# Optimization experiments

Hardware: AMD Instinct MI355X
Metric: run time of the kernel (lower is better)

Reference implementation:

```python
import jax, jax.numpy as jnp
import numpy as np

MARGIN = 0.35


def setup_inputs() -> dict:
    key = jax.random.key(0)
    k1, k2 = jax.random.split(key)
    N, D = 8192, 512
    inp = jax.random.normal(k1, (N, D), dtype=jnp.float32)
    label = jax.random.randint(k2, (N,), 0, D, dtype=jnp.int64)
    return {"input": inp, "label": label}


def reference(input, label):
    N = input.shape[0]
    # Faithful to the torch code: squared-norm terms use L2-normalized input,
    # but the -2*x@x.T cross term uses the UNnormalized input (original quirk).
    x_norm = input / jnp.linalg.norm(input, axis=1, keepdims=True)
    sq = jnp.sum(x_norm * x_norm, axis=1, keepdims=True)  # [N,1]
    dist = sq + sq.T - 2.0 * (input @ input.T)            # [N,N]
    mask = label[:, None] == label[None, :]               # same-label mask
    neg_inf = jnp.array(-jnp.inf, dist.dtype)
    pos_inf = jnp.array(jnp.inf, dist.dtype)
    # hardest positive (max over same-label), hardest negative (min over diff-label)
    positive_part = jnp.max(jnp.where(mask, dist, neg_inf), axis=1)
    negative_part = jnp.min(jnp.where(mask, pos_inf, dist), axis=1)
    triplet = jnp.mean(jnp.maximum(positive_part - negative_part + MARGIN, 0.0))
    # cross entropy: input are logits, label class indices
    logz = jax.nn.logsumexp(input, axis=1)
    true_logit = jnp.take_along_axis(input, label[:, None].astype(jnp.int32), axis=1)[:, 0]
    ce = jnp.mean(logz - true_logit)
    return triplet + ce
```

## Files before the change

kernel.cpp:

```cpp
#include <hip/hip_runtime.h>
#include <hip/hip_bf16.h>
#include <stdint.h>

#define N_ROWS 8192
#define DIM 512
#define NLAB 512
#define MARGIN_F 0.35f
#define NBLK 64
#define NPURE 1953
#define NDIAG 127
#define NTILE (NPURE + NDIAG)
#define ROWSTAT_BLOCKS (N_ROWS / 4)

typedef __attribute__((ext_vector_type(4))) float floatx4;
typedef __attribute__((ext_vector_type(16))) float floatx16;
typedef __attribute__((ext_vector_type(8))) int intx8;

__device__ __forceinline__ unsigned enc_f(float f) {
    unsigned u = __float_as_uint(f);
    return (u & 0x80000000u) ? ~u : (u | 0x80000000u);
}
__device__ __forceinline__ float dec_f(unsigned e) {
    unsigned u = (e & 0x80000000u) ? (e ^ 0x80000000u) : ~e;
    return __uint_as_float(u);
}

__device__ __forceinline__ void load_lds16(const void* g, void* l) {
    __builtin_amdgcn_global_load_lds((__attribute__((address_space(1))) void*)(void*)g,
                                     (__attribute__((address_space(3))) void*)l, 16, 0, 0);
}

__global__ __launch_bounds__(512) void histscan_kernel(const int* __restrict__ label,
                                                       int* __restrict__ offsetArr,
                                                       int* __restrict__ cnt,
                                                       float* __restrict__ out) {
    __shared__ int h[NLAB];
    __shared__ int sc[NLAB];
    int t = threadIdx.x;
    h[t] = 0;
    __syncthreads();
    for (int i = t; i < N_ROWS; i += 512) atomicAdd(&h[label[i]], 1);
    __syncthreads();
    int v = h[t];
    sc[t] = v;
    __syncthreads();
    for (int d = 1; d < NLAB; d <<= 1) {
        int add = (t >= d) ? sc[t - d] : 0;
        __syncthreads();
        sc[t] += add;
        __syncthreads();
    }
    offsetArr[t] = sc[t] - v;
    cnt[t] = 0;
    if (t == 0) out[0] = 0.f;
}

__global__ __launch_bounds__(256) void rowstats_kernel(const float* __restrict__ x,
                                                       const int* __restrict__ label,
                                                       const int* __restrict__ offsetArr,
                                                       int* __restrict__ cnt,
                                                       unsigned char* __restrict__ a8,
                                                       int* __restrict__ sortedLabel,
                                                       float* __restrict__ cePartial,
                                                       unsigned* __restrict__ minEnc,
                                                       unsigned* __restrict__ maxEnc) {
    int gid = blockIdx.x * 256 + threadIdx.x;
    if (gid < N_ROWS) { minEnc[gid] = 0xFFFFFFFFu; maxEnc[gid] = 0u; }

    int w = threadIdx.x >> 6;
    int row = blockIdx.x * 4 + w;
    int l = threadIdx.x & 63;
    const float* xr = x + (size_t)row * DIM;
    float4 v0 = ((const float4*)xr)[2 * l];
    float4 v1 = ((const float4*)xr)[2 * l + 1];
    float vals[8] = {v0.x, v0.y, v0.z, v0.w, v1.x, v1.y, v1.z, v1.w};

    float mx = vals[0];
#pragma unroll
    for (int i = 1; i < 8; i++) mx = fmaxf(mx, vals[i]);
#pragma unroll
    for (int s = 1; s < 64; s <<= 1) mx = fmaxf(mx, __shfl_xor(mx, s, 64));

    float se = 0.f;
#pragma unroll
    for (int i = 0; i < 8; i++) se += expf(vals[i] - mx);
#pragma unroll
    for (int s = 1; s < 64; s <<= 1) se += __shfl_xor(se, s, 64);

    int pos = 0;
    if (l == 0) {
        int lab = label[row];
        pos = offsetArr[lab] + atomicAdd(&cnt[lab], 1);
        sortedLabel[pos] = lab;
    }
    pos = __shfl(pos, 0, 64);

    int w0 = __builtin_amdgcn_cvt_pk_fp8_f32(vals[0], vals[1], 0, false);
    w0 = __builtin_amdgcn_cvt_pk_fp8_f32(vals[2], vals[3], w0, true);
    int w1 = __builtin_amdgcn_cvt_pk_fp8_f32(vals[4], vals[5], 0, false);
    w1 = __builtin_amdgcn_cvt_pk_fp8_f32(vals[6], vals[7], w1, true);
    ((uint2*)(a8 + (size_t)pos * DIM))[l] = make_uint2((unsigned)w0, (unsigned)w1);

    __shared__ float wsum[4];
    if (l == 0) {
        float tl = xr[label[row]];
        wsum[w] = mx + logf(se) - tl;
    }
    __syncthreads();
    if (threadIdx.x == 0)
        cePartial[blockIdx.x] = wsum[0] + wsum[1] + wsum[2] + wsum[3];
}

__global__ __launch_bounds__(256, 4) void gemm_kernel(const unsigned char* __restrict__ A,
                                                      const int* __restrict__ sortedLabel,
                                                      unsigned* __restrict__ minEnc,
                                                      unsigned* __restrict__ maxEnc) {
    __shared__ unsigned char As[2][128 * 64];
    __shared__ unsigned char Bs[2][128 * 64];
    __shared__ float redA[128][2], redB[128][2];
    __shared__ float redImn[128][2], redJmn[128][2];
    __shared__ int labi[128], labj[128];

    int b = blockIdx.x;
    bool diag = (b < NDIAG);
    int bi, bj;
    if (diag) {
        bi = (b < 64) ? b : (b - 63);
        bj = (b < 64) ? b : (b - 64);
    } else {
        int p = b - NDIAG;
        int ci = (int)((sqrtf(8.0f * (float)p + 1.0f) - 1.0f) * 0.5f);
        while ((ci + 1) * (ci + 2) / 2 <= p) ci++;
        while (ci * (ci + 1) / 2 > p) ci--;
        bj = p - ci * (ci + 1) / 2;
        bi = ci + 2;
    }
    int ibase = bi * 128, jbase = bj * 128;

    int t = threadIdx.x;
    int w = t >> 6, l = t & 63;
    int wm = w >> 1, wn = w & 1;
    int cl = l & 31;
    int hi = l >> 5;

    if (diag) {
        if (t < 128) labi[t] = sortedLabel[ibase + t];
        else labj[t - 128] = sortedLabel[jbase + t - 128];
    }

    floatx16 acc[2][2];
#pragma unroll
    for (int a = 0; a < 2; a++)
#pragma unroll
        for (int c = 0; c < 2; c++) acc[a][c] = (floatx16)0.f;

    int s0 = t, s1 = t + 256;
    int r0_ = s0 >> 2, r1_ = s1 >> 2;
    int c0_ = (s0 & 3) ^ ((r0_ >> 1) & 3);
    int c1_ = (s1 & 3) ^ ((r1_ >> 1) & 3);
    const unsigned char* srcA0 = A + (size_t)(ibase + r0_) * DIM + c0_ * 16;
    const unsigned char* srcA1 = A + (size_t)(ibase + r1_) * DIM + c1_ * 16;
    const unsigned char* srcB0 = A + (size_t)(jbase + r0_) * DIM + c0_ * 16;
    const unsigned char* srcB1 = A + (size_t)(jbase + r1_) * DIM + c1_ * 16;
    int ldo0 = s0 * 16, ldo1 = s1 * 16;

#define STAGE(KK, BUF)                                      \
    {                                                       \
        load_lds16(srcA0 + (KK) * 64, As[BUF] + ldo0);      \
        load_lds16(srcA1 + (KK) * 64, As[BUF] + ldo1);      \
        load_lds16(srcB0 + (KK) * 64, Bs[BUF] + ldo0);      \
        load_lds16(srcB1 + (KK) * 64, Bs[BUF] + ldo1);      \
    }

    STAGE(0, 0);
    STAGE(1, 1);
    __syncthreads();

#pragma unroll
    for (int kk = 0; kk < 8; kk++) {
        int cur = kk & 1;

        intx8 b0, b1;
        {
            int r = wn * 64 + cl;
            int f = (r >> 1) & 3;
            const int4* rp = (const int4*)(Bs[cur] + r * 64);
            int4 lo = rp[(2 * hi) ^ f];
            int4 h4 = rp[(2 * hi + 1) ^ f];
            b0[0] = lo.x; b0[1] = lo.y; b0[2] = lo.z; b0[3] = lo.w;
            b0[4] = h4.x; b0[5] = h4.y; b0[6] = h4.z; b0[7] = h4.w;
        }
        {
            int r = wn * 64 + 32 + cl;
            int f = (r >> 1) & 3;
            const int4* rp = (const int4*)(Bs[cur] + r * 64);
            int4 lo = rp[(2 * hi) ^ f];
            int4 h4 = rp[(2 * hi + 1) ^ f];
            b1[0] = lo.x; b1[1] = lo.y; b1[2] = lo.z; b1[3] = lo.w;
            b1[4] = h4.x; b1[5] = h4.y; b1[6] = h4.z; b1[7] = h4.w;
        }
#pragma unroll
        for (int tm = 0; tm < 2; tm++) {
            int r = wm * 64 + tm * 32 + cl;
            int f = (r >> 1) & 3;
            const int4* rp = (const int4*)(As[cur] + r * 64);
            int4 lo = rp[(2 * hi) ^ f];
            int4 h4 = rp[(2 * hi + 1) ^ f];
            intx8 a;
            a[0] = lo.x; a[1] = lo.y; a[2] = lo.z; a[3] = lo.w;
            a[4] = h4.x; a[5] = h4.y; a[6] = h4.z; a[7] = h4.w;
            acc[tm][0] = __builtin_amdgcn_mfma_scale_f32_32x32x64_f8f6f4(
                a, b0, acc[tm][0], 0, 0, 0, 0x7F7F7F7F, 0, 0x7F7F7F7F);
            acc[tm][1] = __builtin_amdgcn_mfma_scale_f32_32x32x64_f8f6f4(
                a, b1, acc[tm][1], 0, 0, 0, 0x7F7F7F7F, 0, 0x7F7F7F7F);
        }

        if (kk < 7) {
            __builtin_amdgcn_s_barrier();
            if (kk < 6) STAGE(kk + 2, cur);
            if (kk < 6) {
                asm volatile("s_waitcnt vmcnt(4)" ::: "memory");
            } else {
                asm volatile("s_waitcnt vmcnt(0)" ::: "memory");
            }
            __builtin_amdgcn_sched_barrier(0);
            __builtin_amdgcn_s_barrier();
        }
    }
#undef STAGE

    const float INF = __builtin_inff();
    int rbase = 4 * hi;

    if (!diag) {
        float mxJ0 = -INF, mxJ1 = -INF;
#pragma unroll
        for (int tm = 0; tm < 2; tm++) {
            float rm[16];
#pragma unroll
            for (int r = 0; r < 16; r++) {
                float v0 = acc[tm][0][r], v1 = acc[tm][1][r];
                rm[r] = fmaxf(v0, v1);
                mxJ0 = fmaxf(mxJ0, v0);
                mxJ1 = fmaxf(mxJ1, v1);
            }
#pragma unroll
            for (int r = 0; r < 16; r++)
#pragma unroll
                for (int s = 1; s < 32; s <<= 1)
                    rm[r] = fmaxf(rm[r], __shfl_xor(rm[r], s, 64));
            if (cl == 0) {
#pragma unroll
                for (int r = 0; r < 16; r++)
                    redA[wm * 64 + tm * 32 + (r & 3) + 8 * (r >> 2) + rbase][wn] = rm[r];
            }
        }
        mxJ0 = fmaxf(mxJ0, __shfl_xor(mxJ0, 32, 64));
        mxJ1 = fmaxf(mxJ1, __shfl_xor(mxJ1, 32, 64));
        if (hi == 0) {
            redB[wn * 64 + cl][wm] = mxJ0;
            redB[wn * 64 + 32 + cl][wm] = mxJ1;
        }
        __syncthreads();
        if (t < 128) {
            atomicMax(&maxEnc[ibase + t], enc_f(fmaxf(redA[t][0], redA[t][1])));
            atomicMax(&maxEnc[jbase + t], enc_f(fmaxf(redB[t][0], redB[t][1])));
        }
    } else {
        int jl0 = labj[wn * 64 + cl];
        int jl1 = labj[wn * 64 + 32 + cl];
        float mnJ0 = INF, mnJ1 = INF, mxJ0 = -INF, mxJ1 = -INF;
#pragma unroll
        for (int tm = 0; tm < 2; tm++) {
            float rmn[16], rmx[16];
#pragma unroll
            for (int r = 0; r < 16; r++) {
                int row_l = wm * 64 + tm * 32 + (r & 3) + 8 * (r >> 2) + rbase;
                int il = labi[row_l];
                float v0 = acc[tm][0][r], v1 = acc[tm][1][r];
                bool sm0 = (jl0 == il), sm1 = (jl1 == il);
                float a0 = sm0 ? v0 : INF, d0 = sm0 ? -INF : v0;
                float a1 = sm1 ? v1 : INF, d1 = sm1 ? -INF : v1;
                rmn[r] = fminf(a0, a1);
                rmx[r] = fmaxf(d0, d1);
                mnJ0 = fminf(mnJ0, a0); mxJ0 = fmaxf(mxJ0, d0);
                mnJ1 = fminf(mnJ1, a1); mxJ1 = fmaxf(mxJ1, d1);
            }
#pragma unroll
            for (int r = 0; r < 16; r++)
#pragma unroll
                for (int s = 1; s < 32; s <<= 1) {
                    rmn[r] = fminf(rmn[r], __shfl_xor(rmn[r], s, 64));
                    rmx[r] = fmaxf(rmx[r], __shfl_xor(rmx[r], s, 64));
                }
            if (cl == 0) {
#pragma unroll
                for (int r = 0; r < 16; r++) {
                    int row_l = wm * 64 + tm * 32 + (r & 3) + 8 * (r >> 2) + rbase;
                    redImn[row_l][wn] = rmn[r];
                    redA[row_l][wn] = rmx[r];
                }
            }
        }
        mnJ0 = fminf(mnJ0, __shfl_xor(mnJ0, 32, 64));
        mnJ1 = fminf(mnJ1, __shfl_xor(mnJ1, 32, 64));
        mxJ0 = fmaxf(mxJ0, __shfl_xor(mxJ0, 32, 64));
        mxJ1 = fmaxf(mxJ1, __shfl_xor(mxJ1, 32, 64));
        if (hi == 0) {
            redJmn[wn * 64 + cl][wm] = mnJ0;
            redJmn[wn * 64 + 32 + cl][wm] = mnJ1;
            redB[wn * 64 + cl][wm] = mxJ0;
            redB[wn * 64 + 32 + cl][wm] = mxJ1;
        }
        __syncthreads();
        if (t < 128) {
            atomicMin(&minEnc[ibase + t], enc_f(fminf(redImn[t][0], redImn[t][1])));
            atomicMax(&maxEnc[ibase + t], enc_f(fmaxf(redA[t][0], redA[t][1])));
            atomicMin(&minEnc[jbase + t], enc_f(fminf(redJmn[t][0], redJmn[t][1])));
            atomicMax(&maxEnc[jbase + t], enc_f(fmaxf(redB[t][0], redB[t][1])));
        }
    }
}

__global__ __launch_bounds__(256) void finalize_kernel(const unsigned* __restrict__ minEnc,
                                                       const unsigned* __restrict__ maxEnc,
                                                       const float* __restrict__ cePartial,
                                                       float* __restrict__ out) {
    int gid = blockIdx.x * 256 + threadIdx.x;
    float mn = dec_f(minEnc[gid]);
    float mxv = dec_f(maxEnc[gid]);
    float s = fmaxf(2.0f * (mxv - mn) + MARGIN_F, 0.f);
    if (gid < ROWSTAT_BLOCKS) s += cePartial[gid];
#pragma unroll
    for (int sh = 1; sh < 64; sh <<= 1) s += __shfl_xor(s, sh, 64);
    __shared__ float red[4];
    int w = threadIdx.x >> 6, l = threadIdx.x & 63;
    if (l == 0) red[w] = s;
    __syncthreads();
    if (threadIdx.x == 0)
        atomicAdd(out, (red[0] + red[1] + red[2] + red[3]) * (1.0f / (float)N_ROWS));
}

extern "C" void kernel_launch(void* const* d_in, const int* in_sizes, int n_in,
                              void* d_out, int out_size, void* d_ws, size_t ws_size,
                              hipStream_t stream) {
    const float* x = (const float*)d_in[0];
    const int* label = (const int*)d_in[1];
    float* out = (float*)d_out;

    char* ws = (char*)d_ws;
    unsigned char* a8 = (unsigned char*)ws;
    char* p = ws + (size_t)N_ROWS * DIM;
    unsigned* minEnc = (unsigned*)p;            p += N_ROWS * 4;
    unsigned* maxEnc = (unsigned*)p;            p += N_ROWS * 4;
    float* cePartial = (float*)p;               p += ROWSTAT_BLOCKS * 4;
    int* offsetArr = (int*)p;                   p += NLAB * 4;
    int* cnt = (int*)p;                         p += NLAB * 4;
    int* sortedLabel = (int*)p;                 p += N_ROWS * 4;

    histscan_kernel<<<1, 512, 0, stream>>>(label, offsetArr, cnt, out);
    rowstats_kernel<<<ROWSTAT_BLOCKS, 256, 0, stream>>>(x, label, offsetArr, cnt, a8,
                                                        sortedLabel, cePartial, minEnc, maxEnc);
    gemm_kernel<<<NTILE, 256, 0, stream>>>(a8, sortedLabel, minEnc, maxEnc);
    finalize_kernel<<<32, 256, 0, stream>>>(minEnc, maxEnc, cePartial, out);
}
```

Measured before the change: 114.7 us.

## Map GEMM tiles to XCDs by super-block and use a 128-byte swizzled LDS layout

Block IDs are remapped so each of the eight XCDs (selected by blockIdx mod 8) works on a contiguous 16x16 super-block of the lower-triangular tile space, which is meant to improve L2 reuse of A and B rows within each XCD. Six XCDs take off-diagonal square super-blocks and two take the four triangular diagonal super-blocks. The grid is padded to 2176 blocks, and the surplus blocks exit early. The LDS layout now packs two 64-byte rows per 128-byte line with an XOR swizzle over 8 chunks, aiming to cut bank conflicts on fragment reads. The diagonal flag is now computed as bi-bj<=1, so the near-diagonal handling stays consistent with the earlier code.

```diff
diff --git a/kernel.cpp b/kernel.cpp
--- a/kernel.cpp
+++ b/kernel.cpp
@@ -7,9 +7,9 @@
 #define NLAB 512
 #define MARGIN_F 0.35f
 #define NBLK 64
-#define NPURE 1953
 #define NDIAG 127
-#define NTILE (NPURE + NDIAG)
+#define NTILE 2080
+#define GEMM_GRID 2176
 #define ROWSTAT_BLOCKS (N_ROWS / 4)
 
 typedef __attribute__((ext_vector_type(4))) float floatx4;
@@ -122,19 +122,25 @@
     __shared__ int labi[128], labj[128];
 
     int b = blockIdx.x;
-    bool diag = (b < NDIAG);
+    int xcd = b & 7, rank = b >> 3;
     int bi, bj;
-    if (diag) {
-        bi = (b < 64) ? b : (b - 63);
-        bj = (b < 64) ? b : (b - 64);
+    if (xcd < 6) {
+        if (rank >= 256) return;
+        int sj = (xcd < 3) ? 0 : ((xcd < 5) ? 1 : 2);
+        int si = (xcd < 3) ? (xcd + 1) : ((xcd < 5) ? (xcd - 1) : 3);
+        bi = si * 16 + (rank >> 4);
+        bj = sj * 16 + (rank & 15);
     } else {
-        int p = b - NDIAG;
-        int ci = (int)((sqrtf(8.0f * (float)p + 1.0f) - 1.0f) * 0.5f);
-        while ((ci + 1) * (ci + 2) / 2 <= p) ci++;
-        while (ci * (ci + 1) / 2 > p) ci--;
-        bj = p - ci * (ci + 1) / 2;
-        bi = ci + 2;
-    }
+        int s = (xcd - 6) * 2 + (rank >= 136 ? 1 : 0);
+        int e = rank - (rank >= 136 ? 136 : 0);
+        int r = (int)((sqrtf(8.0f * (float)e + 1.0f) - 1.0f) * 0.5f);
+        while ((r + 1) * (r + 2) / 2 <= e) r++;
+        while (r * (r + 1) / 2 > e) r--;
+        int c = e - r * (r + 1) / 2;
+        bi = s * 16 + r;
+        bj = s * 16 + c;
+    }
+    bool diag = (bi - bj <= 1);
     int ibase = bi * 128, jbase = bj * 128;
 
     int t = threadIdx.x;
@@ -155,9 +161,10 @@
         for (int c = 0; c < 2; c++) acc[a][c] = (floatx16)0.f;
 
     int s0 = t, s1 = t + 256;
-    int r0_ = s0 >> 2, r1_ = s1 >> 2;
-    int c0_ = (s0 & 3) ^ ((r0_ >> 1) & 3);
-    int c1_ = (s1 & 3) ^ ((r1_ >> 1) & 3);
+    int ln0 = s0 >> 3, u0s = (s0 & 7) ^ (ln0 & 7);
+    int ln1 = s1 >> 3, u1s = (s1 & 7) ^ (ln1 & 7);
+    int r0_ = 2 * ln0 + (u0s >> 2), c0_ = u0s & 3;
+    int r1_ = 2 * ln1 + (u1s >> 2), c1_ = u1s & 3;
     const unsigned char* srcA0 = A + (size_t)(ibase + r0_) * DIM + c0_ * 16;
     const unsigned char* srcA1 = A + (size_t)(ibase + r1_) * DIM + c1_ * 16;
     const unsigned char* srcB0 = A + (size_t)(jbase + r0_) * DIM + c0_ * 16;
@@ -172,6 +179,18 @@
         load_lds16(srcB1 + (KK) * 64, Bs[BUF] + ldo1);      \
     }
 
+#define READ_FRAG(V, TILE, RR)                                      \
+    {                                                               \
+        int R_ = (RR);                                              \
+        int line_ = R_ >> 1, g_ = line_ & 7;                        \
+        int u_ = (R_ & 1) * 4 + 2 * hi;                             \
+        const int4* rp_ = (const int4*)((TILE) + line_ * 128);      \
+        int4 lo_ = rp_[u_ ^ g_];                                    \
+        int4 h4_ = rp_[(u_ + 1) ^ g_];                              \
+        V[0] = lo_.x; V[1] = lo_.y; V[2] = lo_.z; V[3] = lo_.w;     \
+        V[4] = h4_.x; V[5] = h4_.y; V[6] = h4_.z; V[7] = h4_.w;     \
+    }
+
     STAGE(0, 0);
     STAGE(1, 1);
     __syncthreads();
@@ -181,34 +200,12 @@
         int cur = kk & 1;
 
         intx8 b0, b1;
-        {
-            int r = wn * 64 + cl;
-            int f = (r >> 1) & 3;
-            const int4* rp = (const int4*)(Bs[cur] + r * 64);
-            int4 lo = rp[(2 * hi) ^ f];
-            int4 h4 = rp[(2 * hi + 1) ^ f];
-            b0[0] = lo.x; b0[1] = lo.y; b0[2] = lo.z; b0[3] = lo.w;
-            b0[4] = h4.x; b0[5] = h4.y; b0[6] = h4.z; b0[7] = h4.w;
-        }
-        {
-            int r = wn * 64 + 32 + cl;
-            int f = (r >> 1) & 3;
-            const int4* rp = (const int4*)(Bs[cur] + r * 64);
-            int4 lo = rp[(2 * hi) ^ f];
-            int4 h4 = rp[(2 * hi + 1) ^ f];
-            b1[0] = lo.x; b1[1] = lo.y; b1[2] = lo.z; b1[3] = lo.w;
-            b1[4] = h4.x; b1[5] = h4.y; b1[6] = h4.z; b1[7] = h4.w;
-        }
+        READ_FRAG(b0, Bs[cur], wn * 64 + cl);
+        READ_FRAG(b1, Bs[cur], wn * 64 + 32 + cl);
 #pragma unroll
         for (int tm = 0; tm < 2; tm++) {
-            int r = wm * 64 + tm * 32 + cl;
-            int f = (r >> 1) & 3;
-            const int4* rp = (const int4*)(As[cur] + r * 64);
-            int4 lo = rp[(2 * hi) ^ f];
-            int4 h4 = rp[(2 * hi + 1) ^ f];
             intx8 a;
-            a[0] = lo.x; a[1] = lo.y; a[2] = lo.z; a[3] = lo.w;
-            a[4] = h4.x; a[5] = h4.y; a[6] = h4.z; a[7] = h4.w;
+            READ_FRAG(a, As[cur], wm * 64 + tm * 32 + cl);
             acc[tm][0] = __builtin_amdgcn_mfma_scale_f32_32x32x64_f8f6f4(
                 a, b0, acc[tm][0], 0, 0, 0, 0x7F7F7F7F, 0, 0x7F7F7F7F);
             acc[tm][1] = __builtin_amdgcn_mfma_scale_f32_32x32x64_f8f6f4(
@@ -228,6 +225,7 @@
         }
     }
 #undef STAGE
+#undef READ_FRAG
 
     const float INF = __builtin_inff();
     int rbase = 4 * hi;
@@ -361,6 +359,6 @@
     histscan_kernel<<<1, 512, 0, stream>>>(label, offsetArr, cnt, out);
     rowstats_kernel<<<ROWSTAT_BLOCKS, 256, 0, stream>>>(x, label, offsetArr, cnt, a8,
                                                         sortedLabel, cePartial, minEnc, maxEnc);
-    gemm_kernel<<<NTILE, 256, 0, stream>>>(a8, sortedLabel, minEnc, maxEnc);
+    gemm_kernel<<<GEMM_GRID, 256, 0, stream>>>(a8, sortedLabel, minEnc, maxEnc);
     finalize_kernel<<<32, 256, 0, stream>>>(minEnc, maxEnc, cePartial, out);
 }
```

Measured after the change: 140.9 us. 1.23x slower.

## Replace global atomic min/max with per-tile partial buffers reduced in finalize

Applied to the files above, without the earlier changes.

Global atomicMin/atomicMax on order-preserving encoded floats are replaced by plain stores into a partial-result buffer indexed by the block column (64 partials per row for max, 3 neighbouring-block slots for min). The finalize kernel then reduces the 64 max partials and up to 3 min partials per row. This removes atomic contention and the min/max init stores in rowstats. The cost is a larger workspace and more global reads in finalize. Correctness depends on every (row, block) slot being written, and on the label sort confining negatives to neighbouring blocks.

```diff
diff --git a/kernel.cpp b/kernel.cpp
--- a/kernel.cpp
+++ b/kernel.cpp
@@ -16,15 +16,6 @@
 typedef __attribute__((ext_vector_type(16))) float floatx16;
 typedef __attribute__((ext_vector_type(8))) int intx8;
 
-__device__ __forceinline__ unsigned enc_f(float f) {
-    unsigned u = __float_as_uint(f);
-    return (u & 0x80000000u) ? ~u : (u | 0x80000000u);
-}
-__device__ __forceinline__ float dec_f(unsigned e) {
-    unsigned u = (e & 0x80000000u) ? (e ^ 0x80000000u) : ~e;
-    return __uint_as_float(u);
-}
-
 __device__ __forceinline__ void load_lds16(const void* g, void* l) {
     __builtin_amdgcn_global_load_lds((__attribute__((address_space(1))) void*)(void*)g,
                                      (__attribute__((address_space(3))) void*)l, 16, 0, 0);
@@ -61,12 +52,7 @@
                                                        int* __restrict__ cnt,
                                                        unsigned char* __restrict__ a8,
                                                        int* __restrict__ sortedLabel,
-                                                       float* __restrict__ cePartial,
-                                                       unsigned* __restrict__ minEnc,
-                                                       unsigned* __restrict__ maxEnc) {
-    int gid = blockIdx.x * 256 + threadIdx.x;
-    if (gid < N_ROWS) { minEnc[gid] = 0xFFFFFFFFu; maxEnc[gid] = 0u; }
-
+                                                       float* __restrict__ cePartial) {
     int w = threadIdx.x >> 6;
     int row = blockIdx.x * 4 + w;
     int l = threadIdx.x & 63;
@@ -113,8 +99,8 @@
 
 __global__ __launch_bounds__(256, 4) void gemm_kernel(const unsigned char* __restrict__ A,
                                                       const int* __restrict__ sortedLabel,
-                                                      unsigned* __restrict__ minEnc,
-                                                      unsigned* __restrict__ maxEnc) {
+                                                      float* __restrict__ maxP,
+                                                      float* __restrict__ minP) {
     __shared__ unsigned char As[2][128 * 64];
     __shared__ unsigned char Bs[2][128 * 64];
     __shared__ float redA[128][2], redB[128][2];
@@ -262,10 +248,11 @@
             redB[wn * 64 + 32 + cl][wm] = mxJ1;
         }
         __syncthreads();
-        if (t < 128) {
-            atomicMax(&maxEnc[ibase + t], enc_f(fmaxf(redA[t][0], redA[t][1])));
-            atomicMax(&maxEnc[jbase + t], enc_f(fmaxf(redB[t][0], redB[t][1])));
-        }
+        if (t < 128)
+            maxP[(size_t)bj * N_ROWS + ibase + t] = fmaxf(redA[t][0], redA[t][1]);
+        else
+            maxP[(size_t)bi * N_ROWS + jbase + t - 128] =
+                fmaxf(redB[t - 128][0], redB[t - 128][1]);
     } else {
         int jl0 = labj[wn * 64 + cl];
         int jl1 = labj[wn * 64 + 32 + cl];
@@ -313,23 +300,41 @@
             redB[wn * 64 + 32 + cl][wm] = mxJ1;
         }
         __syncthreads();
-        if (t < 128) {
-            atomicMin(&minEnc[ibase + t], enc_f(fminf(redImn[t][0], redImn[t][1])));
-            atomicMax(&maxEnc[ibase + t], enc_f(fmaxf(redA[t][0], redA[t][1])));
-            atomicMin(&minEnc[jbase + t], enc_f(fminf(redJmn[t][0], redJmn[t][1])));
-            atomicMax(&maxEnc[jbase + t], enc_f(fmaxf(redB[t][0], redB[t][1])));
-        }
-    }
-}
-
-__global__ __launch_bounds__(256) void finalize_kernel(const unsigned* __restrict__ minEnc,
-                                                       const unsigned* __restrict__ maxEnc,
+        if (bi == bj) {
+            if (t < 128) {
+                maxP[(size_t)bi * N_ROWS + ibase + t] =
+                    fmaxf(fmaxf(redA[t][0], redA[t][1]), fmaxf(redB[t][0], redB[t][1]));
+                minP[1 * N_ROWS + ibase + t] =
+                    fminf(fminf(redImn[t][0], redImn[t][1]),
+                          fminf(redJmn[t][0], redJmn[t][1]));
+            }
+        } else {
+            if (t < 128) {
+                maxP[(size_t)bj * N_ROWS + ibase + t] = fmaxf(redA[t][0], redA[t][1]);
+                minP[0 * N_ROWS + ibase + t] = fminf(redImn[t][0], redImn[t][1]);
+            } else {
+                int u = t - 128;
+                maxP[(size_t)bi * N_ROWS + jbase + u] = fmaxf(redB[u][0], redB[u][1]);
+                minP[2 * N_ROWS + jbase + u] = fminf(redJmn[u][0], redJmn[u][1]);
+            }
+        }
+    }
+}
+
+__global__ __launch_bounds__(256) void finalize_kernel(const float* __restrict__ maxP,
+                                                       const float* __restrict__ minP,
                                                        const float* __restrict__ cePartial,
                                                        float* __restrict__ out) {
     int gid = blockIdx.x * 256 + threadIdx.x;
-    float mn = dec_f(minEnc[gid]);
-    float mxv = dec_f(maxEnc[gid]);
-    float s = fmaxf(2.0f * (mxv - mn) + MARGIN_F, 0.f);
+    int bi = gid >> 7;
+    const float INF = __builtin_inff();
+    float m = -INF;
+#pragma unroll
+    for (int o = 0; o < 64; o++) m = fmaxf(m, maxP[(size_t)o * N_ROWS + gid]);
+    float mn = minP[1 * N_ROWS + gid];
+    if (bi > 0)  mn = fminf(mn, minP[0 * N_ROWS + gid]);
+    if (bi < 63) mn = fminf(mn, minP[2 * N_ROWS + gid]);
+    float s = fmaxf(2.0f * (m - mn) + MARGIN_F, 0.f);
     if (gid < ROWSTAT_BLOCKS) s += cePartial[gid];
 #pragma unroll
     for (int sh = 1; sh < 64; sh <<= 1) s += __shfl_xor(s, sh, 64);
@@ -351,8 +356,8 @@
     char* ws = (char*)d_ws;
     unsigned char* a8 = (unsigned char*)ws;
     char* p = ws + (size_t)N_ROWS * DIM;
-    unsigned* minEnc = (unsigned*)p;            p += N_ROWS * 4;
-    unsigned* maxEnc = (unsigned*)p;            p += N_ROWS * 4;
+    float* maxP = (float*)p;                    p += (size_t)NBLK * N_ROWS * 4;
+    float* minP = (float*)p;                    p += (size_t)3 * N_ROWS * 4;
     float* cePartial = (float*)p;               p += ROWSTAT_BLOCKS * 4;
     int* offsetArr = (int*)p;                   p += NLAB * 4;
     int* cnt = (int*)p;                         p += NLAB * 4;
@@ -360,7 +365,7 @@
 
     histscan_kernel<<<1, 512, 0, stream>>>(label, offsetArr, cnt, out);
     rowstats_kernel<<<ROWSTAT_BLOCKS, 256, 0, stream>>>(x, label, offsetArr, cnt, a8,
-                                                        sortedLabel, cePartial, minEnc, maxEnc);
-    gemm_kernel<<<NTILE, 256, 0, stream>>>(a8, sortedLabel, minEnc, maxEnc);
-    finalize_kernel<<<32, 256, 0, stream>>>(minEnc, maxEnc, cePartial, out);
-}
+                                                        sortedLabel, cePartial);
+    gemm_kernel<<<NTILE, 256, 0, stream>>>(a8, sortedLabel, maxP, minP);
+    finalize_kernel<<<32, 256, 0, stream>>>(maxP, minP, cePartial, out);
+}
```

Result: slower. 118.8 us (+3.6%).
